# Kernel tuning notes

Hardware: AMD Instinct MI355X
Metric: run time of the kernel (lower is better)

The kernel has to match this reference:

```python
import jax, jax.numpy as jnp
import numpy as np

B, D, F, H = 4096, 1024, 1024, 8


def setup_inputs() -> dict:
    key = jax.random.key(0)
    k1, k2, k3, k4 = jax.random.split(key, 4)
    inputs = jax.random.normal(k1, (B, D), dtype=jnp.float32)
    indices = jax.random.randint(k2, (B,), 0, H, dtype=jnp.int64)
    # lecun_normal-like scale for kernel; zeros bias per flax defaults, but use
    # small random bias so gradients are nontrivial
    kernel = jax.random.normal(k3, (H, D, F), dtype=jnp.float32) / np.sqrt(D)
    bias = jax.random.normal(k4, (H, F), dtype=jnp.float32) * 0.01
    return {"inputs": inputs, "indices": indices, "kernel": kernel, "bias": bias}


def reference(inputs, indices, kernel, bias):
    # Original: per-example gather of kernel[idx] ([D,F]) then x[idx] @ w + b.
    # Equivalent math, vectorized: compute all heads densely then select the
    # routed head per example (avoids materializing a [B,D,F] gathered tensor).
    y = jnp.einsum("bd,hdf->bhf", inputs, kernel) + bias[None, :, :]  # [B,H,F]
    return y[jnp.arange(inputs.shape[0]), indices]  # [B,F]
```

## Files before the change

### kernel.cpp

```cpp
#include <hip/hip_runtime.h>


typedef __attribute__((ext_vector_type(8))) short bf16x8;
typedef __attribute__((ext_vector_type(4))) float f32x4;

#define WAITV(N) asm volatile("s_waitcnt vmcnt(" #N ")" ::: "memory")

static __device__ __forceinline__ unsigned short f2bf(float f) {
  union { float f; unsigned int u; } c; c.f = f;
  unsigned int u = c.u;
  return (unsigned short)((u + 0x7fffu + ((u >> 16) & 1u)) >> 16);
}

static __device__ __forceinline__ void gload16(const void* g, void* s) {
  __builtin_amdgcn_global_load_lds(
      (const __attribute__((address_space(1))) void*)g,
      (__attribute__((address_space(3))) void*)s, 16, 0, 0);
}

__global__ __launch_bounds__(256) void k_prep(
    const float* __restrict__ W, const int* __restrict__ idx,
    unsigned short* __restrict__ Wt, int* __restrict__ cnt,
    int* __restrict__ base8, int* __restrict__ rows) {
  const int bid = blockIdx.x;
  const int t = threadIdx.x;

  if (bid >= 2048) {
    __shared__ int sc[256][8];
    int myi[16];
#pragma unroll
    for (int i = 0; i < 4; ++i) {
      const int4 v = *(const int4*)(idx + t * 16 + i * 4);
      myi[i * 4 + 0] = v.x; myi[i * 4 + 1] = v.y;
      myi[i * 4 + 2] = v.z; myi[i * 4 + 3] = v.w;
    }
    int c[8];
#pragma unroll
    for (int h = 0; h < 8; ++h) c[h] = 0;
#pragma unroll
    for (int e = 0; e < 16; ++e)
#pragma unroll
      for (int h = 0; h < 8; ++h) c[h] += (myi[e] == h) ? 1 : 0;

    int val[8];
#pragma unroll
    for (int h = 0; h < 8; ++h) { val[h] = c[h]; sc[t][h] = c[h]; }
    __syncthreads();
    for (int off = 1; off < 256; off <<= 1) {
      int nb[8];
#pragma unroll
      for (int h = 0; h < 8; ++h) nb[h] = (t >= off) ? sc[t - off][h] : 0;
      __syncthreads();
#pragma unroll
      for (int h = 0; h < 8; ++h) { val[h] += nb[h]; sc[t][h] = val[h]; }
      __syncthreads();
    }
    int tot[8], excl[8];
#pragma unroll
    for (int h = 0; h < 8; ++h) tot[h] = sc[255][h];
#pragma unroll
    for (int h = 0; h < 8; ++h) excl[h] = val[h] - c[h];
    int bases[9];
    bases[0] = 0;
#pragma unroll
    for (int h = 0; h < 7; ++h) bases[h + 1] = (bases[h] + tot[h] + 7) & ~7;
    bases[8] = bases[7] + tot[7];
#pragma unroll
    for (int h = 0; h < 8; ++h) {
      int pos = bases[h] + excl[h];
#pragma unroll
      for (int e = 0; e < 16; ++e) {
        if (myi[e] == h) { rows[pos] = t * 16 + e; ++pos; }
      }
    }
    if (t < 56) {
      const int hh = t >> 3, j = t & 7;
      const int pos = bases[hh] + tot[hh] + j;
      if (pos < bases[hh + 1]) rows[pos] = 0;
    }
    if (t < 128) {
      const int pos = bases[8] + t;
      if (pos < 4160) rows[pos] = 0;
    }
    if (t < 8) cnt[t] = tot[t];
    if (t == 0) {
#pragma unroll
      for (int h = 0; h < 9; ++h) base8[h] = bases[h];
    }
    return;
  }

  __shared__ unsigned short tile[64][68];
  const int h = bid >> 8;
  const int rem = bid & 255;
  const int d0 = (rem >> 4) << 6;
  const int f0 = (rem & 15) << 6;
  const int c4 = (t & 15) * 4;
  const int r0 = t >> 4;
#pragma unroll
  for (int i = 0; i < 4; ++i) {
    const int r = r0 + i * 16;
    const float4 v = *(const float4*)(W + (size_t)(h * 1024 + d0 + r) * 1024 + f0 + c4);
    tile[r][c4 + 0] = f2bf(v.x);
    tile[r][c4 + 1] = f2bf(v.y);
    tile[r][c4 + 2] = f2bf(v.z);
    tile[r][c4 + 3] = f2bf(v.w);
  }
  __syncthreads();
  const int chunk = c4 >> 3;
  const int half = (c4 >> 2) & 1;
#pragma unroll
  for (int i = 0; i < 4; ++i) {
    const int fr = r0 + i * 16;
    const int frow = f0 + fr;
    ushort4 o;
    o.x = tile[c4 + 0][fr];
    o.y = tile[c4 + 1][fr];
    o.z = tile[c4 + 2][fr];
    o.w = tile[c4 + 3][fr];
    const int cS = chunk ^ (frow & 7);
    *(ushort4*)((char*)Wt + (size_t)(h * 1024 + frow) * 2048 +
                (d0 << 1) + (cS << 4) + (half << 3)) = o;
  }
}

__global__ __launch_bounds__(256) void k_gather(
    const float* __restrict__ X, const int* __restrict__ rows,
    unsigned short* __restrict__ Ap) {
  const int slot = blockIdx.x;
  const int b = rows[slot];
  const int t = threadIdx.x;
  const float4 v = *(const float4*)(X + (size_t)b * 1024 + t * 4);
  ushort4 o;
  o.x = f2bf(v.x); o.y = f2bf(v.y); o.z = f2bf(v.z); o.w = f2bf(v.w);
  const int g = t >> 4;
  const int cS = ((t >> 1) & 7) ^ (slot & 7);
  *(ushort4*)((char*)Ap + (size_t)slot * 2048 + (g << 7) + (cS << 4) +
              ((t & 1) << 3)) = o;
}

__global__ __launch_bounds__(256) void k_gemm(
    const unsigned short* __restrict__ Ap, const unsigned short* __restrict__ Wt,
    const int* __restrict__ rows, const int* __restrict__ cnt,
    const int* __restrict__ base8,
    const float* __restrict__ bias, float* __restrict__ out) {
  __shared__ __align__(16) unsigned short As[2][128 * 64];
  __shared__ __align__(16) unsigned short Bs[2][64 * 64];

  const int blk = blockIdx.x;
  const int h = blk & 7;
  const int nt = (blk >> 3) & 15;
  const int mt = blk >> 7;

  const int cnt_h = cnt[h];
  const int basep = base8[h];
  const int m0 = mt * 128;
  if (m0 >= cnt_h) return;
  const int n0 = nt * 64;

  const int t = threadIdx.x;
  const int lane = t & 63;
  const int wave = t >> 6;
  const int wr = wave >> 1, wc = wave & 1;

  const int srow = t >> 3;
  const int scol = (t & 7) << 4;
  const char* aRow[4];
  const char* bRow[2];
#pragma unroll
  for (int r = 0; r < 4; ++r) {
    int ar = basep + m0 + r * 32 + srow;
    ar = ar < 4223 ? ar : 4223;
    aRow[r] = (const char*)Ap + (size_t)ar * 2048 + scol;
  }
#pragma unroll
  for (int r = 0; r < 2; ++r)
    bRow[r] = (const char*)Wt + (size_t)(h * 1024 + n0 + r * 32 + srow) * 2048 + scol;

  f32x4 acc[4][2];
#pragma unroll
  for (int m = 0; m < 4; ++m)
#pragma unroll
    for (int n = 0; n < 2; ++n)
      acc[m][n] = (f32x4){0.f, 0.f, 0.f, 0.f};

  auto stage = [&](int s, int k0) {
#pragma unroll
    for (int r = 0; r < 4; ++r)
      gload16(aRow[r] + k0 * 2, (char*)(&As[s][0]) + r * 4096 + t * 16);
#pragma unroll
    for (int r = 0; r < 2; ++r)
      gload16(bRow[r] + k0 * 2, (char*)(&Bs[s][0]) + r * 4096 + t * 16);
  };

  const int swz = (lane & 7) << 4;
  const int ra = (wr * 64 + (lane & 15)) * 128;
  const int rb = (wc * 32 + (lane & 15)) * 128;
  const int kc = (lane >> 4) << 4;

  auto compute = [&](int s) {
    const char* ab = (const char*)(&As[s][0]);
    const char* bb = (const char*)(&Bs[s][0]);
#pragma unroll
    for (int ksub = 0; ksub < 2; ++ksub) {
      const int co = ((ksub * 64) + kc) ^ swz;
      bf16x8 af[4], bfr[2];
#pragma unroll
      for (int a = 0; a < 4; ++a)
        af[a] = *(const bf16x8*)(ab + ra + a * 2048 + co);
#pragma unroll
      for (int b = 0; b < 2; ++b)
        bfr[b] = *(const bf16x8*)(bb + rb + b * 2048 + co);
#pragma unroll
      for (int a = 0; a < 4; ++a)
#pragma unroll
        for (int b = 0; b < 2; ++b)
          acc[a][b] = __builtin_amdgcn_mfma_f32_16x16x32_bf16(af[a], bfr[b], acc[a][b], 0, 0, 0);
    }
  };

  stage(0, 0);
  stage(1, 64);

  for (int ts = 0; ts < 14; ++ts) {
    WAITV(6);
    __builtin_amdgcn_s_barrier();
    __builtin_amdgcn_sched_barrier(0);
    compute(ts & 1);
    __builtin_amdgcn_s_barrier();
    __builtin_amdgcn_sched_barrier(0);
    stage(ts & 1, (ts + 2) * 64);
    __builtin_amdgcn_sched_barrier(0);
  }
  WAITV(6);
  __builtin_amdgcn_s_barrier();
  __builtin_amdgcn_sched_barrier(0);
  compute(0);
  WAITV(0);
  __builtin_amdgcn_s_barrier();
  __builtin_amdgcn_sched_barrier(0);
  compute(1);

  int rmap[4][4];
  bool vld[4][4];
#pragma unroll
  for (int m = 0; m < 4; ++m) {
#pragma unroll
    for (int j = 0; j < 4; ++j) {
      const int lr = wr * 64 + m * 16 + (lane >> 4) * 4 + j;
      const bool v = (m0 + lr) < cnt_h;
      vld[m][j] = v;
      rmap[m][j] = v ? rows[basep + m0 + lr] : 0;
    }
  }
#pragma unroll
  for (int n = 0; n < 2; ++n) {
    const int c = n0 + wc * 32 + n * 16 + (lane & 15);
    const float bv = bias[h * 1024 + c];
#pragma unroll
    for (int m = 0; m < 4; ++m) {
#pragma unroll
      for (int j = 0; j < 4; ++j) {
        if (vld[m][j])
          out[(size_t)rmap[m][j] * 1024 + c] = acc[m][n][j] + bv;
      }
    }
  }
}

extern "C" void kernel_launch(void* const* d_in, const int* in_sizes, int n_in,
                              void* d_out, int out_size, void* d_ws, size_t ws_size,
                              hipStream_t stream) {
  const float* X = (const float*)d_in[0];
  const int* idx = (const int*)d_in[1];
  const float* W = (const float*)d_in[2];
  const float* bias = (const float*)d_in[3];
  float* out = (float*)d_out;

  char* ws = (char*)d_ws;
  int* cnt = (int*)ws;
  int* base8 = (int*)(ws + 64);
  int* rows = (int*)(ws + 256);
  unsigned short* Wt = (unsigned short*)(ws + 32768);
  unsigned short* Ap = (unsigned short*)(ws + 32768 + 16777216);

  k_prep<<<dim3(2049), 256, 0, stream>>>(W, idx, Wt, cnt, base8, rows);
  k_gather<<<dim3(4160), 256, 0, stream>>>(X, rows, Ap);
  k_gemm<<<dim3(8 * 16 * 16), 256, 0, stream>>>(Ap, Wt, rows, cnt, base8, bias, out);
}
```

Before: 47.31 us.

## Shrink GEMM M-tile to 64 and triple-buffer LDS with one barrier per step

The routed GEMM tile shrinks from 128x64 to 64x64, roughly doubling the number of non-empty blocks so the 256 compute units get more parallel work. The double-buffered loop, which had two barriers per k-step, becomes a three-buffer ring. Each step prefetches two tiles ahead and needs only one barrier. In exchange, each block does less data reuse per load, and the fixed grid now covers only 1024 rows per head, which relies on the per-head counts staying below that.

```diff
diff --git a/kernel.cpp b/kernel.cpp
--- a/kernel.cpp
+++ b/kernel.cpp
@@ -144,8 +144,8 @@
     const int* __restrict__ rows, const int* __restrict__ cnt,
     const int* __restrict__ base8,
     const float* __restrict__ bias, float* __restrict__ out) {
-  __shared__ __align__(16) unsigned short As[2][128 * 64];
-  __shared__ __align__(16) unsigned short Bs[2][64 * 64];
+  __shared__ __align__(16) unsigned short As[3][64 * 64];
+  __shared__ __align__(16) unsigned short Bs[3][64 * 64];
 
   const int blk = blockIdx.x;
   const int h = blk & 7;
@@ -154,7 +154,7 @@
 
   const int cnt_h = cnt[h];
   const int basep = base8[h];
-  const int m0 = mt * 128;
+  const int m0 = mt * 64;
   if (m0 >= cnt_h) return;
   const int n0 = nt * 64;
 
@@ -165,89 +165,76 @@
 
   const int srow = t >> 3;
   const int scol = (t & 7) << 4;
-  const char* aRow[4];
-  const char* bRow[2];
-#pragma unroll
-  for (int r = 0; r < 4; ++r) {
-    int ar = basep + m0 + r * 32 + srow;
-    ar = ar < 4223 ? ar : 4223;
-    aRow[r] = (const char*)Ap + (size_t)ar * 2048 + scol;
-  }
-#pragma unroll
-  for (int r = 0; r < 2; ++r)
-    bRow[r] = (const char*)Wt + (size_t)(h * 1024 + n0 + r * 32 + srow) * 2048 + scol;
-
-  f32x4 acc[4][2];
-#pragma unroll
-  for (int m = 0; m < 4; ++m)
+  int ar0 = basep + m0 + srow;      ar0 = ar0 < 4159 ? ar0 : 4159;
+  int ar1 = basep + m0 + 32 + srow; ar1 = ar1 < 4159 ? ar1 : 4159;
+  const char* aRow0 = (const char*)Ap + (size_t)ar0 * 2048 + scol;
+  const char* aRow1 = (const char*)Ap + (size_t)ar1 * 2048 + scol;
+  const char* bRow0 = (const char*)Wt + (size_t)(h * 1024 + n0 + srow) * 2048 + scol;
+  const char* bRow1 = (const char*)Wt + (size_t)(h * 1024 + n0 + 32 + srow) * 2048 + scol;
+
+  f32x4 acc[2][2];
+#pragma unroll
+  for (int m = 0; m < 2; ++m)
 #pragma unroll
     for (int n = 0; n < 2; ++n)
       acc[m][n] = (f32x4){0.f, 0.f, 0.f, 0.f};
 
-  auto stage = [&](int s, int k0) {
-#pragma unroll
-    for (int r = 0; r < 4; ++r)
-      gload16(aRow[r] + k0 * 2, (char*)(&As[s][0]) + r * 4096 + t * 16);
-#pragma unroll
-    for (int r = 0; r < 2; ++r)
-      gload16(bRow[r] + k0 * 2, (char*)(&Bs[s][0]) + r * 4096 + t * 16);
+  auto stage = [&](char* aDst, char* bDst, int k0) {
+    const int kby = k0 * 2;
+    gload16(aRow0 + kby, aDst + t * 16);
+    gload16(aRow1 + kby, aDst + 4096 + t * 16);
+    gload16(bRow0 + kby, bDst + t * 16);
+    gload16(bRow1 + kby, bDst + 4096 + t * 16);
   };
 
   const int swz = (lane & 7) << 4;
-  const int ra = (wr * 64 + (lane & 15)) * 128;
+  const int ra = (wr * 32 + (lane & 15)) * 128;
   const int rb = (wc * 32 + (lane & 15)) * 128;
   const int kc = (lane >> 4) << 4;
 
-  auto compute = [&](int s) {
-    const char* ab = (const char*)(&As[s][0]);
-    const char* bb = (const char*)(&Bs[s][0]);
+  auto compute = [&](const char* ab, const char* bb) {
 #pragma unroll
     for (int ksub = 0; ksub < 2; ++ksub) {
       const int co = ((ksub * 64) + kc) ^ swz;
-      bf16x8 af[4], bfr[2];
-#pragma unroll
-      for (int a = 0; a < 4; ++a)
-        af[a] = *(const bf16x8*)(ab + ra + a * 2048 + co);
-#pragma unroll
-      for (int b = 0; b < 2; ++b)
-        bfr[b] = *(const bf16x8*)(bb + rb + b * 2048 + co);
-#pragma unroll
-      for (int a = 0; a < 4; ++a)
-#pragma unroll
-        for (int b = 0; b < 2; ++b)
-          acc[a][b] = __builtin_amdgcn_mfma_f32_16x16x32_bf16(af[a], bfr[b], acc[a][b], 0, 0, 0);
+      const bf16x8 a0 = *(const bf16x8*)(ab + ra + co);
+      const bf16x8 a1 = *(const bf16x8*)(ab + ra + 2048 + co);
+      const bf16x8 b0 = *(const bf16x8*)(bb + rb + co);
+      const bf16x8 b1 = *(const bf16x8*)(bb + rb + 2048 + co);
+      acc[0][0] = __builtin_amdgcn_mfma_f32_16x16x32_bf16(a0, b0, acc[0][0], 0, 0, 0);
+      acc[0][1] = __builtin_amdgcn_mfma_f32_16x16x32_bf16(a0, b1, acc[0][1], 0, 0, 0);
+      acc[1][0] = __builtin_amdgcn_mfma_f32_16x16x32_bf16(a1, b0, acc[1][0], 0, 0, 0);
+      acc[1][1] = __builtin_amdgcn_mfma_f32_16x16x32_bf16(a1, b1, acc[1][1], 0, 0, 0);
     }
   };
 
-  stage(0, 0);
-  stage(1, 64);
-
-  for (int ts = 0; ts < 14; ++ts) {
-    WAITV(6);
+  char* a0p = (char*)&As[0][0]; char* a1p = (char*)&As[1][0]; char* a2p = (char*)&As[2][0];
+  char* b0p = (char*)&Bs[0][0]; char* b1p = (char*)&Bs[1][0]; char* b2p = (char*)&Bs[2][0];
+
+  stage(a0p, b0p, 0);
+  stage(a1p, b1p, 64);
+
+  for (int ts = 0; ts < 15; ++ts) {
+    WAITV(4);
     __builtin_amdgcn_s_barrier();
     __builtin_amdgcn_sched_barrier(0);
-    compute(ts & 1);
-    __builtin_amdgcn_s_barrier();
+    if (ts < 14) stage(a2p, b2p, (ts + 2) * 64);
     __builtin_amdgcn_sched_barrier(0);
-    stage(ts & 1, (ts + 2) * 64);
-    __builtin_amdgcn_sched_barrier(0);
-  }
-  WAITV(6);
-  __builtin_amdgcn_s_barrier();
-  __builtin_amdgcn_sched_barrier(0);
-  compute(0);
+    compute(a0p, b0p);
+    char* tA = a0p; a0p = a1p; a1p = a2p; a2p = tA;
+    char* tB = b0p; b0p = b1p; b1p = b2p; b2p = tB;
+  }
   WAITV(0);
   __builtin_amdgcn_s_barrier();
   __builtin_amdgcn_sched_barrier(0);
-  compute(1);
-
-  int rmap[4][4];
-  bool vld[4][4];
-#pragma unroll
-  for (int m = 0; m < 4; ++m) {
+  compute(a0p, b0p);
+
+  int rmap[2][4];
+  bool vld[2][4];
+#pragma unroll
+  for (int m = 0; m < 2; ++m) {
 #pragma unroll
     for (int j = 0; j < 4; ++j) {
-      const int lr = wr * 64 + m * 16 + (lane >> 4) * 4 + j;
+      const int lr = wr * 32 + m * 16 + (lane >> 4) * 4 + j;
       const bool v = (m0 + lr) < cnt_h;
       vld[m][j] = v;
       rmap[m][j] = v ? rows[basep + m0 + lr] : 0;
@@ -258,7 +245,7 @@
     const int c = n0 + wc * 32 + n * 16 + (lane & 15);
     const float bv = bias[h * 1024 + c];
 #pragma unroll
-    for (int m = 0; m < 4; ++m) {
+    for (int m = 0; m < 2; ++m) {
 #pragma unroll
       for (int j = 0; j < 4; ++j) {
         if (vld[m][j])
```

New measurement: 48.90 us. 3.4% more time.
